# Optimization experiments

Hardware: AMD Instinct MI355X
Metric: run time of the kernel (lower is better)

## Reference

```python
import jax, jax.numpy as jnp
import numpy as np

EMB = 300      # node embedding dim (GNNGraph default)
NL = 5         # num GNN layers
G = 4096       # number of graphs in batch
ATOM_F, ATOM_V = 9, 128   # OGB-style atom encoder: 9 categorical feats
BOND_F, BOND_V = 3, 8     # OGB-style bond encoder: 3 categorical feats
BN_EPS = 1e-5


def _bn(x, g, b, m, v):
    # BatchNorm1d in eval mode (running stats)
    return (x - m) * jax.lax.rsqrt(v + BN_EPS) * g + b


def _gnn(x, edge_index, edge_attr, batch,
         atom_emb, bond_emb, vn_emb,
         gin_eps, gin_W1, gin_b1, gin_bn1_g, gin_bn1_b, gin_bn1_m, gin_bn1_v,
         gin_W2, gin_b2, bn_g, bn_b, bn_m, bn_v,
         vn_W1, vn_b1, vn_bn1_g, vn_bn1_b, vn_bn1_m, vn_bn1_v,
         vn_W2, vn_b2, vn_bn2_g, vn_bn2_b, vn_bn2_m, vn_bn2_v):
    N = x.shape[0]
    # AtomEncoder / BondEncoder: sum of per-feature embedding lookups
    h = atom_emb[jnp.arange(ATOM_F)[None, :], x].sum(axis=1)          # [N, EMB]
    e = bond_emb[jnp.arange(BOND_F)[None, :], edge_attr].sum(axis=1)  # [E, EMB]
    row, col = edge_index[0], edge_index[1]
    # virtual node embedding, one per graph
    vn = jnp.broadcast_to(vn_emb[0], (G, EMB))
    for l in range(NL):
        h = h + vn[batch]                                   # broadcast virtual node
        # GINConv: message = relu(x_j + edge_emb), aggr = scatter-add at target
        msg = jax.nn.relu(h[row] + e)                       # [E, EMB]
        agg = jax.ops.segment_sum(msg, col, num_segments=N) # [N, EMB]
        t = (1.0 + gin_eps[l]) * h + agg
        t = jnp.dot(t, gin_W1[l]) + gin_b1[l]               # [N, 2*EMB]
        t = jax.nn.relu(_bn(t, gin_bn1_g[l], gin_bn1_b[l], gin_bn1_m[l], gin_bn1_v[l]))
        t = jnp.dot(t, gin_W2[l]) + gin_b2[l]               # [N, EMB]
        hn = _bn(t, bn_g[l], bn_b[l], bn_m[l], bn_v[l])     # outer BatchNorm
        if l < NL - 1:
            hn = jax.nn.relu(hn)                            # (dropout inactive in eval)
            # virtual node update: global_add_pool(h_list[layer]) + vn -> MLP
            pooled = jax.ops.segment_sum(h, batch, num_segments=G) + vn
            u = jnp.dot(pooled, vn_W1[l]) + vn_b1[l]
            u = jax.nn.relu(_bn(u, vn_bn1_g[l], vn_bn1_b[l], vn_bn1_m[l], vn_bn1_v[l]))
            u = jnp.dot(u, vn_W2[l]) + vn_b2[l]
            vn = jax.nn.relu(_bn(u, vn_bn2_g[l], vn_bn2_b[l], vn_bn2_m[l], vn_bn2_v[l]))
        h = hn
    # global_mean_pool over graphs
    counts = jax.ops.segment_sum(jnp.ones((N,), h.dtype), batch, num_segments=G)
    return jax.ops.segment_sum(h, batch, num_segments=G) / jnp.maximum(counts, 1.0)[:, None]


def setup_inputs() -> dict:
    key = jax.random.key(0)
    ks = iter(jax.random.split(key, 64))
    N, E = 100000, 250000
    d = {}
    d['x'] = jax.random.randint(next(ks), (N, ATOM_F), 0, ATOM_V, dtype=jnp.int32)
    d['edge_index'] = jax.random.randint(next(ks), (2, E), 0, N, dtype=jnp.int32)
    d['edge_attr'] = jax.random.randint(next(ks), (E, BOND_F), 0, BOND_V, dtype=jnp.int32)
    d['batch'] = jnp.sort(jax.random.randint(next(ks), (N,), 0, G, dtype=jnp.int32))
    s = 0.05
    d['atom_emb'] = jax.random.normal(next(ks), (ATOM_F, ATOM_V, EMB), jnp.float32) * s
    d['bond_emb'] = jax.random.normal(next(ks), (BOND_F, BOND_V, EMB), jnp.float32) * s
    d['vn_emb'] = jax.random.normal(next(ks), (1, EMB), jnp.float32) * s
    d['gin_eps'] = jax.random.normal(next(ks), (NL,), jnp.float32) * 0.01
    d['gin_W1'] = jax.random.normal(next(ks), (NL, EMB, 2 * EMB), jnp.float32) * s
    d['gin_b1'] = jax.random.normal(next(ks), (NL, 2 * EMB), jnp.float32) * s
    d['gin_bn1_g'] = 1.0 + jax.random.normal(next(ks), (NL, 2 * EMB), jnp.float32) * s
    d['gin_bn1_b'] = jax.random.normal(next(ks), (NL, 2 * EMB), jnp.float32) * s
    d['gin_bn1_m'] = jax.random.normal(next(ks), (NL, 2 * EMB), jnp.float32) * s
    d['gin_bn1_v'] = jax.random.uniform(next(ks), (NL, 2 * EMB), jnp.float32) + 0.5
    d['gin_W2'] = jax.random.normal(next(ks), (NL, 2 * EMB, EMB), jnp.float32) * s
    d['gin_b2'] = jax.random.normal(next(ks), (NL, EMB), jnp.float32) * s
    d['bn_g'] = 1.0 + jax.random.normal(next(ks), (NL, EMB), jnp.float32) * s
    d['bn_b'] = jax.random.normal(next(ks), (NL, EMB), jnp.float32) * s
    d['bn_m'] = jax.random.normal(next(ks), (NL, EMB), jnp.float32) * s
    d['bn_v'] = jax.random.uniform(next(ks), (NL, EMB), jnp.float32) + 0.5
    V = NL - 1
    d['vn_W1'] = jax.random.normal(next(ks), (V, EMB, 2 * EMB), jnp.float32) * s
    d['vn_b1'] = jax.random.normal(next(ks), (V, 2 * EMB), jnp.float32) * s
    d['vn_bn1_g'] = 1.0 + jax.random.normal(next(ks), (V, 2 * EMB), jnp.float32) * s
    d['vn_bn1_b'] = jax.random.normal(next(ks), (V, 2 * EMB), jnp.float32) * s
    d['vn_bn1_m'] = jax.random.normal(next(ks), (V, 2 * EMB), jnp.float32) * s
    d['vn_bn1_v'] = jax.random.uniform(next(ks), (V, 2 * EMB), jnp.float32) + 0.5
    d['vn_W2'] = jax.random.normal(next(ks), (V, 2 * EMB, EMB), jnp.float32) * s
    d['vn_b2'] = jax.random.normal(next(ks), (V, EMB), jnp.float32) * s
    d['vn_bn2_g'] = 1.0 + jax.random.normal(next(ks), (V, EMB), jnp.float32) * s
    d['vn_bn2_b'] = jax.random.normal(next(ks), (V, EMB), jnp.float32) * s
    d['vn_bn2_m'] = jax.random.normal(next(ks), (V, EMB), jnp.float32) * s
    d['vn_bn2_v'] = jax.random.uniform(next(ks), (V, EMB), jnp.float32) + 0.5
    return d


def reference(x, edge_index, edge_attr, batch,
              atom_emb, bond_emb, vn_emb,
              gin_eps, gin_W1, gin_b1, gin_bn1_g, gin_bn1_b, gin_bn1_m, gin_bn1_v,
              gin_W2, gin_b2, bn_g, bn_b, bn_m, bn_v,
              vn_W1, vn_b1, vn_bn1_g, vn_bn1_b, vn_bn1_m, vn_bn1_v,
              vn_W2, vn_b2, vn_bn2_g, vn_bn2_b, vn_bn2_m, vn_bn2_v):
    return _gnn(x, edge_index, edge_attr, batch,
                atom_emb, bond_emb, vn_emb,
                gin_eps, gin_W1, gin_b1, gin_bn1_g, gin_bn1_b, gin_bn1_m, gin_bn1_v,
                gin_W2, gin_b2, bn_g, bn_b, bn_m, bn_v,
                vn_W1, vn_b1, vn_bn1_g, vn_bn1_b, vn_bn1_m, vn_bn1_v,
                vn_W2, vn_b2, vn_bn2_g, vn_bn2_b, vn_bn2_m, vn_bn2_v)
```

## Files before the change

### kernel.cpp

```cpp
#include <hip/hip_runtime.h>
#include <hip/hip_bf16.h>

#define EMBD 300
#define GG   4096
#define NLAY 5
#define KP1  320
#define KP2  640
#define NP1  640
#define NP2  384
#define WPER (NP1*KP1 + NP2*KP2)

typedef unsigned short ushort_t;
typedef short short8 __attribute__((ext_vector_type(8)));
typedef short short4v __attribute__((ext_vector_type(4)));
typedef float f32x4 __attribute__((ext_vector_type(4)));

static inline int cdiv(int a, int b) { return (a + b - 1) / b; }


__device__ inline void dma16(const ushort_t* g, ushort_t* l) {
    __builtin_amdgcn_global_load_lds(
        (const __attribute__((address_space(1))) unsigned int*)g,
        (__attribute__((address_space(3))) unsigned int*)l, 16, 0, 0);
}

__device__ inline ushort_t bf16_of(float v) {
    union { __hip_bfloat16 b; ushort_t u; } c;
    c.b = __float2bfloat16(v);
    return c.u;
}

__device__ inline float bf2f(ushort_t u) {
    union { unsigned int i; float f; } c;
    c.i = ((unsigned int)u) << 16;
    return c.f;
}


__global__ void atom_encode_bf(const int* __restrict__ x, const float* __restrict__ aemb,
                               ushort_t* __restrict__ h, int N) {
    int i = blockIdx.x * blockDim.x + threadIdx.x;
    int total = N * 75;
    if (i >= total) return;
    int n = i / 75, d4 = i - n * 75;
    const int* xr = x + n * 9;
    float4 s = make_float4(0.f, 0.f, 0.f, 0.f);
    const float4* a4 = (const float4*)aemb;
#pragma unroll
    for (int f = 0; f < 9; ++f) {
        float4 v = a4[(size_t)((f << 7) + xr[f]) * 75 + d4];
        s.x += v.x; s.y += v.y; s.z += v.z; s.w += v.w;
    }
    short4v o;
    o[0] = (short)bf16_of(s.x); o[1] = (short)bf16_of(s.y);
    o[2] = (short)bf16_of(s.z); o[3] = (short)bf16_of(s.w);
    *(short4v*)(h + (size_t)n * KP1 + d4 * 4) = o;
}

__global__ void init_vn4(const float* __restrict__ vn_emb, float* __restrict__ vn) {
    int i = blockIdx.x * blockDim.x + threadIdx.x;
    if (i >= GG * 75) return;
    ((float4*)vn)[i] = ((const float4*)vn_emb)[i % 75];
}

__global__ void find_starts(const int* __restrict__ batch, int* __restrict__ starts, int N) {
    int g = blockIdx.x * blockDim.x + threadIdx.x;
    if (g > GG) return;
    int lo = 0, hi = N;
    while (lo < hi) {
        int mid = (lo + hi) >> 1;
        if (batch[mid] < g) lo = mid + 1; else hi = mid;
    }
    starts[g] = lo;
}

__global__ void bond_combo(const float* __restrict__ bemb, float* __restrict__ ebsum) {
    int i = blockIdx.x * blockDim.x + threadIdx.x;
    if (i >= 512 * EMBD) return;
    int c = i / EMBD, d = i - c * EMBD;
    int a0 = c >> 6, a1 = (c >> 3) & 7, a2 = c & 7;
    ebsum[i] = bemb[a0 * EMBD + d] + bemb[(8 + a1) * EMBD + d] + bemb[(16 + a2) * EMBD + d];
}

__global__ void conv_all(const float* __restrict__ gW1, const float* __restrict__ gW2,
                         const float* __restrict__ vW1, const float* __restrict__ vW2,
                         ushort_t* __restrict__ wh) {
    int i = blockIdx.x * blockDim.x + threadIdx.x;
    int total = WPER * 9;
    if (i >= total) return;
    int mlp = i / WPER, r = i - mlp * WPER;
    const float *W1, *W2;
    if (mlp < NLAY) {
        W1 = gW1 + (size_t)mlp * EMBD * 2 * EMBD;
        W2 = gW2 + (size_t)mlp * 2 * EMBD * EMBD;
    } else {
        int l = mlp - NLAY;
        W1 = vW1 + (size_t)l * EMBD * 2 * EMBD;
        W2 = vW2 + (size_t)l * 2 * EMBD * EMBD;
    }
    float v;
    if (r < NP1 * KP1) {
        int n = r / KP1, k = r - n * KP1;
        v = (n < 2 * EMBD && k < EMBD) ? W1[(size_t)k * (2 * EMBD) + n] : 0.f;
    } else {
        int r2 = r - NP1 * KP1;
        int n = r2 / KP2, k = r2 - n * KP2;
        v = (n < EMBD && k < 2 * EMBD) ? W2[(size_t)k * EMBD + n] : 0.f;
    }
    wh[i] = bf16_of(v);
}


__global__ void ecount(const int* __restrict__ ei, int* __restrict__ cnt, int E) {
    int e = blockIdx.x * blockDim.x + threadIdx.x;
    if (e >= E) return;
    atomicAdd(&cnt[ei[E + e]], 1);
}

__global__ void scan_part(const int* __restrict__ cnt, int* __restrict__ bsum, int N) {
    __shared__ int sh[256];
    int b = blockIdx.x, t = threadIdx.x;
    int base = b * 1024;
    int s = 0;
    for (int j = t; j < 1024; j += 256) {
        int idx = base + j;
        if (idx < N) s += cnt[idx];
    }
    sh[t] = s;
    __syncthreads();
    for (int d = 128; d > 0; d >>= 1) {
        if (t < d) sh[t] += sh[t + d];
        __syncthreads();
    }
    if (t == 0) bsum[b] = sh[0];
}

__global__ void scan_top(int* __restrict__ bsum, int nb) {
    __shared__ int sh[1024];
    int t = threadIdx.x;
    int v = (t < nb) ? bsum[t] : 0;
    sh[t] = v;
    __syncthreads();
    for (int d = 1; d < 1024; d <<= 1) {
        int u = (t >= d) ? sh[t - d] : 0;
        __syncthreads();
        sh[t] += u;
        __syncthreads();
    }
    if (t < nb) bsum[t] = sh[t] - v;
}

__global__ void scan_final(const int* __restrict__ cnt, const int* __restrict__ bsum,
                           int* __restrict__ estart, int* __restrict__ cursor, int N, int E) {
    __shared__ int sh[256];
    int b = blockIdx.x, t = threadIdx.x;
    int base = b * 1024 + t * 4;
    int c[4];
    int s = 0;
#pragma unroll
    for (int j = 0; j < 4; ++j) {
        int idx = base + j;
        c[j] = (idx < N) ? cnt[idx] : 0;
        s += c[j];
    }
    sh[t] = s;
    __syncthreads();
    for (int d = 1; d < 256; d <<= 1) {
        int u = (t >= d) ? sh[t - d] : 0;
        __syncthreads();
        sh[t] += u;
        __syncthreads();
    }
    int run = sh[t] - s + bsum[b];
#pragma unroll
    for (int j = 0; j < 4; ++j) {
        int idx = base + j;
        if (idx < N) { estart[idx] = run; cursor[idx] = run; run += c[j]; }
    }
    if (b == 0 && t == 0) estart[N] = E;
}

__global__ void escatter(const int* __restrict__ ei, const int* __restrict__ ea,
                         int* __restrict__ cursor, int2* __restrict__ epack, int E) {
    int e = blockIdx.x * blockDim.x + threadIdx.x;
    if (e >= E) return;
    int c = ei[E + e];
    int p = atomicAdd(&cursor[c], 1);
    epack[p] = make_int2(ei[e], (ea[3 * e] << 6) | (ea[3 * e + 1] << 3) | ea[3 * e + 2]);
}


__global__ void pool_prep(ushort_t* __restrict__ h, const float* __restrict__ vn,
                          const int* __restrict__ starts, ushort_t* __restrict__ vnaB) {
    int g = blockIdx.x;
    int t = threadIdx.x;
    if (t >= EMBD) return;
    float vng = vn[(size_t)g * EMBD + t];
    int s0 = starts[g], s1 = starts[g + 1];
    float s = 0.f;
    for (int n = s0; n < s1; ++n) {
        size_t idx = (size_t)n * KP1 + t;
        float v = bf2f(h[idx]) + vng;
        h[idx] = bf16_of(v);
        s += v;
    }
    vnaB[(size_t)g * KP1 + t] = bf16_of(s + vng);
}

__global__ void prep_vn(ushort_t* __restrict__ h, const float* __restrict__ vn,
                        const int* __restrict__ batch, int N) {
    int i = blockIdx.x * blockDim.x + threadIdx.x;
    int total = N * 75;
    if (i >= total) return;
    int n = i / 75, d4 = i - n * 75;
    float4 vv = ((const float4*)vn)[(size_t)batch[n] * 75 + d4];
    short4v hv = *(short4v*)(h + (size_t)n * KP1 + d4 * 4);
    short4v o;
    o[0] = (short)bf16_of(bf2f((ushort_t)hv[0]) + vv.x);
    o[1] = (short)bf16_of(bf2f((ushort_t)hv[1]) + vv.y);
    o[2] = (short)bf16_of(bf2f((ushort_t)hv[2]) + vv.z);
    o[3] = (short)bf16_of(bf2f((ushort_t)hv[3]) + vv.w);
    *(short4v*)(h + (size_t)n * KP1 + d4 * 4) = o;
}

__global__ void pool_mean(const ushort_t* __restrict__ h, const int* __restrict__ starts,
                          float* __restrict__ out) {
    int g = blockIdx.x;
    int t = threadIdx.x;
    if (t >= EMBD) return;
    int s0 = starts[g], s1 = starts[g + 1];
    float s = 0.f;
    for (int n = s0; n < s1; ++n) s += bf2f(h[(size_t)n * KP1 + t]);
    float cnt = (float)(s1 - s0);
    out[(size_t)g * EMBD + t] = s / fmaxf(cnt, 1.0f);
}

#define NPB 4

__global__ void aggregate(const ushort_t* __restrict__ h, const float* __restrict__ ebsum,
                          const int* __restrict__ estart, const int2* __restrict__ epack,
                          const float* __restrict__ epsp,
                          ushort_t* __restrict__ aggB, int N) {
    int n = blockIdx.x * NPB + threadIdx.x / 80;
    int slot = threadIdx.x % 80;
    if (n >= N) return;
    float4 acc = make_float4(0.f, 0.f, 0.f, 0.f);
    if (slot < 75) {
        const float4* b4 = (const float4*)ebsum;
        float ce = 1.0f + *epsp;
        short4v hv = *(const short4v*)(h + (size_t)n * KP1 + slot * 4);
        acc.x = ce * bf2f((ushort_t)hv[0]);
        acc.y = ce * bf2f((ushort_t)hv[1]);
        acc.z = ce * bf2f((ushort_t)hv[2]);
        acc.w = ce * bf2f((ushort_t)hv[3]);
        int p0 = estart[n], p1 = estart[n + 1];
        for (int p = p0; p < p1; ++p) {
            int2 ep = epack[p];
            short4v xv = *(const short4v*)(h + (size_t)ep.x * KP1 + slot * 4);
            float4 ev = b4[(size_t)ep.y * 75 + slot];
            acc.x += fmaxf(bf2f((ushort_t)xv[0]) + ev.x, 0.f);
            acc.y += fmaxf(bf2f((ushort_t)xv[1]) + ev.y, 0.f);
            acc.z += fmaxf(bf2f((ushort_t)xv[2]) + ev.z, 0.f);
            acc.w += fmaxf(bf2f((ushort_t)xv[3]) + ev.w, 0.f);
        }
    }
    short4v bv4;
    bv4[0] = (short)bf16_of(acc.x);
    bv4[1] = (short)bf16_of(acc.y);
    bv4[2] = (short)bf16_of(acc.z);
    bv4[3] = (short)bf16_of(acc.w);
    *(short4v*)(aggB + (size_t)n * KP1 + slot * 4) = bv4;
}

#define BMg 128
#define BNg 128

__global__ __launch_bounds__(256) void gemm_as(
    const ushort_t* __restrict__ A, int KP,
    const ushort_t* __restrict__ B,
    const float* __restrict__ bias, const float* __restrict__ gg,
    const float* __restrict__ bb, const float* __restrict__ bm,
    const float* __restrict__ bv,
    int Mc, int NnReal, int relu, int nb, int mb,
    float* __restrict__ outF, int ldF,
    ushort_t* __restrict__ outB, int ldP)
{
    __shared__ ushort_t sA[2][BMg * 32];
    __shared__ ushort_t sB[2][BNg * 32];

    int id = blockIdx.x;
    int hi = id / (8 * nb);
    int rem = id - hi * 8 * nb;
    int xcd = rem & 7;
    int nblk = rem >> 3;
    int mblk = hi * 8 + xcd;
    if (mblk >= mb) return;

    const int tid = threadIdx.x;
    const int lane = tid & 63;
    const int w = tid >> 6;
    const int m0 = mblk * BMg;
    const int n0 = nblk * BNg;
    const int wm = (w & 1) * 64;
    const int wn = (w >> 1) * 64;

    const ushort_t* gA[2];
    const ushort_t* gB[2];
    int lbase[2];
#pragma unroll
    for (int i = 0; i < 2; ++i) {
        int s = tid + 256 * i;
        int m = s >> 2, qp = s & 3;
        int q = (qp - (m >> 1)) & 3;
        int msrc = (m0 + m < Mc) ? (m0 + m) : (Mc - 1);
        gA[i] = A + (size_t)msrc * KP + 8 * q;
        gB[i] = B + (size_t)(n0 + m) * KP + 8 * q;
        lbase[i] = (w * 64 + 256 * i) * 8;
    }

    f32x4 acc[4][4];
#pragma unroll
    for (int a = 0; a < 4; ++a)
#pragma unroll
        for (int b = 0; b < 4; ++b) acc[a][b] = (f32x4)(0.f);

    const int q = lane >> 4;
    const int c16 = lane & 15;
    const int kt = KP >> 5;

#pragma unroll
    for (int i = 0; i < 2; ++i) {
        dma16(gA[i], sA[0] + lbase[i]); gA[i] += 32;
        dma16(gB[i], sB[0] + lbase[i]); gB[i] += 32;
    }
    __syncthreads();

    for (int t = 0; t < kt; ++t) {
        int cur = t & 1, nxt = cur ^ 1;
        if (t + 1 < kt) {
#pragma unroll
            for (int i = 0; i < 2; ++i) {
                dma16(gA[i], sA[nxt] + lbase[i]); gA[i] += 32;
                dma16(gB[i], sB[nxt] + lbase[i]); gB[i] += 32;
            }
        }
        short8 av[4], bhv[4];
#pragma unroll
        for (int tt = 0; tt < 4; ++tt) {
            int m = wm + tt * 16 + c16;
            int q2 = (q + (m >> 1)) & 3;
            av[tt] = *(const short8*)(sA[cur] + m * 32 + q2 * 8);
        }
#pragma unroll
        for (int uu = 0; uu < 4; ++uu) {
            int n = wn + uu * 16 + c16;
            int q2 = (q + (n >> 1)) & 3;
            bhv[uu] = *(const short8*)(sB[cur] + n * 32 + q2 * 8);
        }
#pragma unroll
        for (int tt = 0; tt < 4; ++tt)
#pragma unroll
            for (int uu = 0; uu < 4; ++uu)
                acc[tt][uu] = __builtin_amdgcn_mfma_f32_16x16x32_bf16(av[tt], bhv[uu], acc[tt][uu], 0, 0, 0);
        __syncthreads();
    }

#pragma unroll
    for (int uu = 0; uu < 4; ++uu) {
        int gn = n0 + wn + uu * 16 + c16;
        float sc = 0.f, sh = 0.f;
        if (gn < NnReal) {
            sc = gg[gn] * rsqrtf(bv[gn] + 1e-5f);
            sh = bb[gn] + (bias[gn] - bm[gn]) * sc;
        }
#pragma unroll
        for (int tt = 0; tt < 4; ++tt) {
            int rbase = m0 + wm + tt * 16 + q * 4;
#pragma unroll
            for (int r = 0; r < 4; ++r) {
                int gm = rbase + r;
                if (gm >= Mc) continue;
                float y = acc[tt][uu][r] * sc + sh;
                if (relu) y = fmaxf(y, 0.f);
                if (outF) {
                    if (gn < NnReal) outF[(size_t)gm * ldF + gn] = y;
                } else {
                    if (gn < ldP) outB[(size_t)gm * ldP + gn] = bf16_of(y);
                }
            }
        }
    }
}


struct MlpP {
    const float *b1, *g1, *be1, *m1, *v1;
    const float *b2, *g2, *be2, *m2, *v2;
};

static void run_mlp(hipStream_t stream, const ushort_t* inB, int M,
                    const ushort_t* wh, int mlp,
                    ushort_t* tB, int CH,
                    const MlpP& W, ushort_t* outB, int relu2) {
    const ushort_t* w1 = wh + (size_t)mlp * WPER;
    const ushort_t* w2 = w1 + NP1 * KP1;
    for (int c0 = 0; c0 < M; c0 += CH) {
        int Mc = (M - c0 < CH) ? (M - c0) : CH;
        int mb = cdiv(Mc, BMg);
        int mbp = cdiv(mb, 8) * 8;
        {
            int nb = NP1 / BNg;
            gemm_as<<<nb * mbp, 256, 0, stream>>>(
                inB + (size_t)c0 * KP1, KP1, w1,
                W.b1, W.g1, W.be1, W.m1, W.v1,
                Mc, 2 * EMBD, 1, nb, mb,
                nullptr, 0, tB, KP2);
        }
        {
            int nb = NP2 / BNg;
            gemm_as<<<nb * mbp, 256, 0, stream>>>(
                tB, KP2, w2,
                W.b2, W.g2, W.be2, W.m2, W.v2,
                Mc, EMBD, relu2, nb, mb,
                nullptr, 0, outB + (size_t)c0 * KP1, KP1);
        }
    }
}


extern "C" void kernel_launch(void* const* d_in, const int* in_sizes, int n_in,
                              void* d_out, int out_size, void* d_ws, size_t ws_size,
                              hipStream_t stream) {
    const int*   x        = (const int*)d_in[0];
    const int*   ei       = (const int*)d_in[1];
    const int*   ea       = (const int*)d_in[2];
    const int*   batch    = (const int*)d_in[3];
    const float* atom_emb = (const float*)d_in[4];
    const float* bond_emb = (const float*)d_in[5];
    const float* vn_emb   = (const float*)d_in[6];
    const float* gin_eps  = (const float*)d_in[7];
    const float* gin_W1   = (const float*)d_in[8];
    const float* gin_b1   = (const float*)d_in[9];
    const float* gin_bn1g = (const float*)d_in[10];
    const float* gin_bn1b = (const float*)d_in[11];
    const float* gin_bn1m = (const float*)d_in[12];
    const float* gin_bn1v = (const float*)d_in[13];
    const float* gin_W2   = (const float*)d_in[14];
    const float* gin_b2   = (const float*)d_in[15];
    const float* bn_g     = (const float*)d_in[16];
    const float* bn_b     = (const float*)d_in[17];
    const float* bn_m     = (const float*)d_in[18];
    const float* bn_v     = (const float*)d_in[19];
    const float* vn_W1    = (const float*)d_in[20];
    const float* vn_b1    = (const float*)d_in[21];
    const float* vn_bn1g  = (const float*)d_in[22];
    const float* vn_bn1b  = (const float*)d_in[23];
    const float* vn_bn1m  = (const float*)d_in[24];
    const float* vn_bn1v  = (const float*)d_in[25];
    const float* vn_W2    = (const float*)d_in[26];
    const float* vn_b2    = (const float*)d_in[27];
    const float* vn_bn2g  = (const float*)d_in[28];
    const float* vn_bn2b  = (const float*)d_in[29];
    const float* vn_bn2m  = (const float*)d_in[30];
    const float* vn_bn2v  = (const float*)d_in[31];

    const int N = in_sizes[3];
    const int E = in_sizes[1] / 2;
    const int NB = cdiv(N, 1024);

    char* base = (char*)d_ws;
    size_t off = 0;
    ushort_t* hbuf = (ushort_t*)(base + off); off += (size_t)N * KP1 * 2;
    ushort_t* aggB = (ushort_t*)(base + off); off += (size_t)N * KP1 * 2;
    float* vnbuf   = (float*)(base + off);    off += (size_t)GG * EMBD * 4;
    int*   starts  = (int*)(base + off);      off += 4104 * 4;
    int*   cnt     = (int*)(base + off);      off += (size_t)N * 4;
    int*   cursor  = (int*)(base + off);      off += (size_t)N * 4;
    int*   estart  = (int*)(base + off);      off += ((size_t)N + 8) * 4;
    int*   bsum    = (int*)(base + off);      off += 1032 * 4;
    int2*  epack   = (int2*)(base + off);     off += (size_t)E * 8;
    float* ebsum   = (float*)(base + off);    off += (size_t)512 * EMBD * 4;
    ushort_t* whA  = (ushort_t*)(base + off); off += (size_t)9 * WPER * 2;
    ushort_t* vnaB = (ushort_t*)(base + off); off += (size_t)GG * KP1 * 2;
    off = (off + 255) & ~(size_t)255;

    size_t avail = (ws_size > off) ? ws_size - off : 0;
    int CH = (int)(avail / (KP2 * 2));
    CH &= ~255;
    if (CH > N) CH = (N + 255) & ~255;
    else if (CH >= (N + 1) / 2) CH = (((N + 1) / 2) + 255) & ~255;
    if (CH < 2048) CH = 2048;
    ushort_t* tB = (ushort_t*)(base + off);

    const int BLK = 256;
    int ne4 = N * 75;

    find_starts<<<cdiv(GG + 1, BLK), BLK, 0, stream>>>(batch, starts, N);
    atom_encode_bf<<<cdiv(ne4, BLK), BLK, 0, stream>>>(x, atom_emb, hbuf, N);
    init_vn4<<<cdiv(GG * 75, BLK), BLK, 0, stream>>>(vn_emb, vnbuf);
    bond_combo<<<cdiv(512 * EMBD, BLK), BLK, 0, stream>>>(bond_emb, ebsum);
    conv_all<<<cdiv(9 * WPER, BLK), BLK, 0, stream>>>(gin_W1, gin_W2, vn_W1, vn_W2, whA);
    hipMemsetAsync(cnt, 0, (size_t)N * 4, stream);
    hipMemsetAsync(vnaB, 0, (size_t)GG * KP1 * 2, stream);
    ecount<<<cdiv(E, BLK), BLK, 0, stream>>>(ei, cnt, E);
    scan_part<<<NB, 256, 0, stream>>>(cnt, bsum, N);
    scan_top<<<1, 1024, 0, stream>>>(bsum, NB);
    scan_final<<<NB, 256, 0, stream>>>(cnt, bsum, estart, cursor, N, E);
    escatter<<<cdiv(E, BLK), BLK, 0, stream>>>(ei, ea, cursor, epack, E);

    for (int l = 0; l < NLAY; ++l) {
        int last = (l == NLAY - 1);

        if (!last)
            pool_prep<<<GG, 320, 0, stream>>>(hbuf, vnbuf, starts, vnaB);
        else
            prep_vn<<<cdiv(ne4, BLK), BLK, 0, stream>>>(hbuf, vnbuf, batch, N);

        aggregate<<<cdiv(N, NPB), NPB * 80, 0, stream>>>(
            hbuf, ebsum, estart, epack, gin_eps + l, aggB, N);

        MlpP Wn = { gin_b1 + (size_t)l * 2 * EMBD,
                    gin_bn1g + (size_t)l * 2 * EMBD, gin_bn1b + (size_t)l * 2 * EMBD,
                    gin_bn1m + (size_t)l * 2 * EMBD, gin_bn1v + (size_t)l * 2 * EMBD,
                    gin_b2 + (size_t)l * EMBD,
                    bn_g + (size_t)l * EMBD, bn_b + (size_t)l * EMBD,
                    bn_m + (size_t)l * EMBD, bn_v + (size_t)l * EMBD };
        run_mlp(stream, aggB, N, whA, l, tB, CH, Wn, hbuf, last ? 0 : 1);

        if (!last) {
            MlpP Wv = { vn_b1 + (size_t)l * 2 * EMBD,
                        vn_bn1g + (size_t)l * 2 * EMBD, vn_bn1b + (size_t)l * 2 * EMBD,
                        vn_bn1m + (size_t)l * 2 * EMBD, vn_bn1v + (size_t)l * 2 * EMBD,
                        vn_b2 + (size_t)l * EMBD,
                        vn_bn2g + (size_t)l * EMBD, vn_bn2b + (size_t)l * EMBD,
                        vn_bn2m + (size_t)l * EMBD, vn_bn2v + (size_t)l * EMBD };
            const ushort_t* w1 = whA + (size_t)(NLAY + l) * WPER;
            const ushort_t* w2 = w1 + NP1 * KP1;
            int mb = cdiv(GG, BMg), mbp = cdiv(mb, 8) * 8;
            gemm_as<<<(NP1 / BNg) * mbp, 256, 0, stream>>>(
                vnaB, KP1, w1,
                Wv.b1, Wv.g1, Wv.be1, Wv.m1, Wv.v1,
                GG, 2 * EMBD, 1, NP1 / BNg, mb,
                nullptr, 0, tB, KP2);
            gemm_as<<<(NP2 / BNg) * mbp, 256, 0, stream>>>(
                tB, KP2, w2,
                Wv.b2, Wv.g2, Wv.be2, Wv.m2, Wv.v2,
                GG, EMBD, 1, NP2 / BNg, mb,
                vnbuf, EMBD, nullptr, 0);
        }
    }

    pool_mean<<<GG, 320, 0, stream>>>(hbuf, starts, (float*)d_out);
}
```

Baseline: 1.933 ms.

## Fuse two-layer MLP GEMMs into one kernel and fold virtual-node add into epilogue

```diff
diff --git a/kernel.cpp b/kernel.cpp
--- a/kernel.cpp
+++ b/kernel.cpp
@@ -38,13 +38,14 @@
 
 
 __global__ void atom_encode_bf(const int* __restrict__ x, const float* __restrict__ aemb,
+                               const float* __restrict__ vn_emb,
                                ushort_t* __restrict__ h, int N) {
     int i = blockIdx.x * blockDim.x + threadIdx.x;
     int total = N * 75;
     if (i >= total) return;
     int n = i / 75, d4 = i - n * 75;
     const int* xr = x + n * 9;
-    float4 s = make_float4(0.f, 0.f, 0.f, 0.f);
+    float4 s = ((const float4*)vn_emb)[d4];
     const float4* a4 = (const float4*)aemb;
 #pragma unroll
     for (int f = 0; f < 9; ++f) {
@@ -190,37 +191,15 @@
 }
 
 
-__global__ void pool_prep(ushort_t* __restrict__ h, const float* __restrict__ vn,
+__global__ void pool_only(const ushort_t* __restrict__ h, const float* __restrict__ vn,
                           const int* __restrict__ starts, ushort_t* __restrict__ vnaB) {
     int g = blockIdx.x;
     int t = threadIdx.x;
     if (t >= EMBD) return;
-    float vng = vn[(size_t)g * EMBD + t];
     int s0 = starts[g], s1 = starts[g + 1];
     float s = 0.f;
-    for (int n = s0; n < s1; ++n) {
-        size_t idx = (size_t)n * KP1 + t;
-        float v = bf2f(h[idx]) + vng;
-        h[idx] = bf16_of(v);
-        s += v;
-    }
-    vnaB[(size_t)g * KP1 + t] = bf16_of(s + vng);
-}
-
-__global__ void prep_vn(ushort_t* __restrict__ h, const float* __restrict__ vn,
-                        const int* __restrict__ batch, int N) {
-    int i = blockIdx.x * blockDim.x + threadIdx.x;
-    int total = N * 75;
-    if (i >= total) return;
-    int n = i / 75, d4 = i - n * 75;
-    float4 vv = ((const float4*)vn)[(size_t)batch[n] * 75 + d4];
-    short4v hv = *(short4v*)(h + (size_t)n * KP1 + d4 * 4);
-    short4v o;
-    o[0] = (short)bf16_of(bf2f((ushort_t)hv[0]) + vv.x);
-    o[1] = (short)bf16_of(bf2f((ushort_t)hv[1]) + vv.y);
-    o[2] = (short)bf16_of(bf2f((ushort_t)hv[2]) + vv.z);
-    o[3] = (short)bf16_of(bf2f((ushort_t)hv[3]) + vv.w);
-    *(short4v*)(h + (size_t)n * KP1 + d4 * 4) = o;
+    for (int n = s0; n < s1; ++n) s += bf2f(h[(size_t)n * KP1 + t]);
+    vnaB[(size_t)g * KP1 + t] = bf16_of(s + vn[(size_t)g * EMBD + t]);
 }
 
 __global__ void pool_mean(const ushort_t* __restrict__ h, const int* __restrict__ starts,
@@ -272,159 +251,147 @@
     *(short4v*)(aggB + (size_t)n * KP1 + slot * 4) = bv4;
 }
 
-#define BMg 128
-#define BNg 128
-
-__global__ __launch_bounds__(256) void gemm_as(
-    const ushort_t* __restrict__ A, int KP,
-    const ushort_t* __restrict__ B,
-    const float* __restrict__ bias, const float* __restrict__ gg,
-    const float* __restrict__ bb, const float* __restrict__ bm,
-    const float* __restrict__ bv,
-    int Mc, int NnReal, int relu, int nb, int mb,
-    float* __restrict__ outF, int ldF,
-    ushort_t* __restrict__ outB, int ldP)
+
+__global__ __launch_bounds__(256, 2) void fused_mlp(
+    const ushort_t* __restrict__ A,
+    const ushort_t* __restrict__ W1,
+    const ushort_t* __restrict__ W2,
+    const float* __restrict__ b1, const float* __restrict__ g1,
+    const float* __restrict__ bb1, const float* __restrict__ bm1, const float* __restrict__ bv1,
+    const float* __restrict__ b2, const float* __restrict__ g2,
+    const float* __restrict__ bb2, const float* __restrict__ bm2, const float* __restrict__ bv2,
+    int M, int relu2,
+    const float* __restrict__ vnadd, const int* __restrict__ batch,
+    ushort_t* __restrict__ outB,
+    float* __restrict__ outF)
 {
-    __shared__ ushort_t sA[2][BMg * 32];
-    __shared__ ushort_t sB[2][BNg * 32];
-
-    int id = blockIdx.x;
-    int hi = id / (8 * nb);
-    int rem = id - hi * 8 * nb;
-    int xcd = rem & 7;
-    int nblk = rem >> 3;
-    int mblk = hi * 8 + xcd;
-    if (mblk >= mb) return;
+    __shared__ ushort_t sA[10 * 64 * 32];
+    __shared__ ushort_t tL[64 * 136];
 
     const int tid = threadIdx.x;
     const int lane = tid & 63;
     const int w = tid >> 6;
-    const int m0 = mblk * BMg;
-    const int n0 = nblk * BNg;
-    const int wm = (w & 1) * 64;
-    const int wn = (w >> 1) * 64;
-
-    const ushort_t* gA[2];
-    const ushort_t* gB[2];
-    int lbase[2];
-#pragma unroll
-    for (int i = 0; i < 2; ++i) {
-        int s = tid + 256 * i;
-        int m = s >> 2, qp = s & 3;
-        int q = (qp - (m >> 1)) & 3;
-        int msrc = (m0 + m < Mc) ? (m0 + m) : (Mc - 1);
-        gA[i] = A + (size_t)msrc * KP + 8 * q;
-        gB[i] = B + (size_t)(n0 + m) * KP + 8 * q;
-        lbase[i] = (w * 64 + 256 * i) * 8;
-    }
-
-    f32x4 acc[4][4];
-#pragma unroll
-    for (int a = 0; a < 4; ++a)
-#pragma unroll
-        for (int b = 0; b < 4; ++b) acc[a][b] = (f32x4)(0.f);
-
+    const int m0 = blockIdx.x * 64;
     const int q = lane >> 4;
     const int c16 = lane & 15;
-    const int kt = KP >> 5;
-
-#pragma unroll
-    for (int i = 0; i < 2; ++i) {
-        dma16(gA[i], sA[0] + lbase[i]); gA[i] += 32;
-        dma16(gB[i], sB[0] + lbase[i]); gB[i] += 32;
+
+    {
+        int m = tid >> 2, qp = tid & 3;
+        int q0 = (qp - (m >> 1)) & 3;
+        int msrc = m0 + m; if (msrc >= M) msrc = M - 1;
+        const ushort_t* gA = A + (size_t)msrc * KP1 + 8 * q0;
+        int lb = w * 512;
+#pragma unroll
+        for (int kt = 0; kt < 10; ++kt)
+            dma16(gA + kt * 32, sA + kt * 2048 + lb);
     }
     __syncthreads();
 
-    for (int t = 0; t < kt; ++t) {
-        int cur = t & 1, nxt = cur ^ 1;
-        if (t + 1 < kt) {
-#pragma unroll
-            for (int i = 0; i < 2; ++i) {
-                dma16(gA[i], sA[nxt] + lbase[i]); gA[i] += 32;
-                dma16(gB[i], sB[nxt] + lbase[i]); gB[i] += 32;
+    f32x4 acc2[4][6];
+#pragma unroll
+    for (int a = 0; a < 4; ++a)
+#pragma unroll
+        for (int b = 0; b < 6; ++b) acc2[a][b] = (f32x4)(0.f);
+
+    for (int c = 0; c < 5; ++c) {
+        float sc1[2], sh1[2];
+#pragma unroll
+        for (int uu = 0; uu < 2; ++uu) {
+            int col = c * 128 + w * 32 + uu * 16 + c16;
+            if (col < 2 * EMBD) {
+                float s = g1[col] * rsqrtf(bv1[col] + 1e-5f);
+                sc1[uu] = s;
+                sh1[uu] = bb1[col] + (b1[col] - bm1[col]) * s;
+            } else { sc1[uu] = 0.f; sh1[uu] = 0.f; }
+        }
+        f32x4 acc1[4][2];
+#pragma unroll
+        for (int a = 0; a < 4; ++a) { acc1[a][0] = (f32x4)(0.f); acc1[a][1] = (f32x4)(0.f); }
+        for (int kt = 0; kt < 10; ++kt) {
+            short8 bf[2];
+#pragma unroll
+            for (int uu = 0; uu < 2; ++uu) {
+                int ncol = c * 128 + w * 32 + uu * 16 + c16;
+                bf[uu] = *(const short8*)(W1 + (size_t)ncol * KP1 + kt * 32 + q * 8);
             }
-        }
-        short8 av[4], bhv[4];
-#pragma unroll
-        for (int tt = 0; tt < 4; ++tt) {
-            int m = wm + tt * 16 + c16;
-            int q2 = (q + (m >> 1)) & 3;
-            av[tt] = *(const short8*)(sA[cur] + m * 32 + q2 * 8);
-        }
-#pragma unroll
-        for (int uu = 0; uu < 4; ++uu) {
-            int n = wn + uu * 16 + c16;
-            int q2 = (q + (n >> 1)) & 3;
-            bhv[uu] = *(const short8*)(sB[cur] + n * 32 + q2 * 8);
-        }
-#pragma unroll
-        for (int tt = 0; tt < 4; ++tt)
-#pragma unroll
-            for (int uu = 0; uu < 4; ++uu)
-                acc[tt][uu] = __builtin_amdgcn_mfma_f32_16x16x32_bf16(av[tt], bhv[uu], acc[tt][uu], 0, 0, 0);
-        __syncthreads();
-    }
-
-#pragma unroll
-    for (int uu = 0; uu < 4; ++uu) {
-        int gn = n0 + wn + uu * 16 + c16;
-        float sc = 0.f, sh = 0.f;
-        if (gn < NnReal) {
-            sc = gg[gn] * rsqrtf(bv[gn] + 1e-5f);
-            sh = bb[gn] + (bias[gn] - bm[gn]) * sc;
-        }
-#pragma unroll
-        for (int tt = 0; tt < 4; ++tt) {
-            int rbase = m0 + wm + tt * 16 + q * 4;
-#pragma unroll
-            for (int r = 0; r < 4; ++r) {
-                int gm = rbase + r;
-                if (gm >= Mc) continue;
-                float y = acc[tt][uu][r] * sc + sh;
-                if (relu) y = fmaxf(y, 0.f);
-                if (outF) {
-                    if (gn < NnReal) outF[(size_t)gm * ldF + gn] = y;
+            short8 af[4];
+#pragma unroll
+            for (int tt = 0; tt < 4; ++tt) {
+                int m2 = tt * 16 + c16;
+                int q2 = (q + (m2 >> 1)) & 3;
+                af[tt] = *(const short8*)(sA + kt * 2048 + m2 * 32 + q2 * 8);
+            }
+#pragma unroll
+            for (int tt = 0; tt < 4; ++tt)
+#pragma unroll
+                for (int uu = 0; uu < 2; ++uu)
+                    acc1[tt][uu] = __builtin_amdgcn_mfma_f32_16x16x32_bf16(af[tt], bf[uu], acc1[tt][uu], 0, 0, 0);
+        }
+#pragma unroll
+        for (int uu = 0; uu < 2; ++uu) {
+            int col = w * 32 + uu * 16 + c16;
+#pragma unroll
+            for (int tt = 0; tt < 4; ++tt)
+#pragma unroll
+                for (int r = 0; r < 4; ++r) {
+                    int row = tt * 16 + q * 4 + r;
+                    float y = fmaxf(acc1[tt][uu][r] * sc1[uu] + sh1[uu], 0.f);
+                    tL[row * 136 + col] = bf16_of(y);
+                }
+        }
+        __syncthreads();
+        for (int kt2 = 0; kt2 < 4; ++kt2) {
+            short8 bf2[6];
+#pragma unroll
+            for (int uu = 0; uu < 6; ++uu) {
+                int ncol = w * 96 + uu * 16 + c16;
+                bf2[uu] = *(const short8*)(W2 + (size_t)ncol * KP2 + c * 128 + kt2 * 32 + q * 8);
+            }
+            short8 af2[4];
+#pragma unroll
+            for (int tt = 0; tt < 4; ++tt) {
+                int m2 = tt * 16 + c16;
+                af2[tt] = *(const short8*)(tL + m2 * 136 + kt2 * 32 + q * 8);
+            }
+#pragma unroll
+            for (int tt = 0; tt < 4; ++tt)
+#pragma unroll
+                for (int uu = 0; uu < 6; ++uu)
+                    acc2[tt][uu] = __builtin_amdgcn_mfma_f32_16x16x32_bf16(af2[tt], bf2[uu], acc2[tt][uu], 0, 0, 0);
+        }
+        __syncthreads();
+    }
+
+    float sc2[6], sh2[6];
+#pragma unroll
+    for (int uu = 0; uu < 6; ++uu) {
+        int gn = w * 96 + uu * 16 + c16;
+        if (gn < EMBD) {
+            float s = g2[gn] * rsqrtf(bv2[gn] + 1e-5f);
+            sc2[uu] = s;
+            sh2[uu] = bb2[gn] + (b2[gn] - bm2[gn]) * s;
+        } else { sc2[uu] = 0.f; sh2[uu] = 0.f; }
+    }
+#pragma unroll
+    for (int tt = 0; tt < 4; ++tt)
+#pragma unroll
+        for (int r = 0; r < 4; ++r) {
+            int gm = m0 + tt * 16 + q * 4 + r;
+            if (gm >= M) continue;
+            const float* vrow = vnadd ? (vnadd + (size_t)batch[gm] * EMBD) : nullptr;
+#pragma unroll
+            for (int uu = 0; uu < 6; ++uu) {
+                int gn = w * 96 + uu * 16 + c16;
+                float y = acc2[tt][uu][r] * sc2[uu] + sh2[uu];
+                if (relu2) y = fmaxf(y, 0.f);
+                if (vrow && gn < EMBD) y += vrow[gn];
+                if (outB) {
+                    if (gn < KP1) outB[(size_t)gm * KP1 + gn] = bf16_of(y);
                 } else {
-                    if (gn < ldP) outB[(size_t)gm * ldP + gn] = bf16_of(y);
+                    if (gn < EMBD) outF[(size_t)gm * EMBD + gn] = y;
                 }
             }
         }
-    }
-}
-
-
-struct MlpP {
-    const float *b1, *g1, *be1, *m1, *v1;
-    const float *b2, *g2, *be2, *m2, *v2;
-};
-
-static void run_mlp(hipStream_t stream, const ushort_t* inB, int M,
-                    const ushort_t* wh, int mlp,
-                    ushort_t* tB, int CH,
-                    const MlpP& W, ushort_t* outB, int relu2) {
-    const ushort_t* w1 = wh + (size_t)mlp * WPER;
-    const ushort_t* w2 = w1 + NP1 * KP1;
-    for (int c0 = 0; c0 < M; c0 += CH) {
-        int Mc = (M - c0 < CH) ? (M - c0) : CH;
-        int mb = cdiv(Mc, BMg);
-        int mbp = cdiv(mb, 8) * 8;
-        {
-            int nb = NP1 / BNg;
-            gemm_as<<<nb * mbp, 256, 0, stream>>>(
-                inB + (size_t)c0 * KP1, KP1, w1,
-                W.b1, W.g1, W.be1, W.m1, W.v1,
-                Mc, 2 * EMBD, 1, nb, mb,
-                nullptr, 0, tB, KP2);
-        }
-        {
-            int nb = NP2 / BNg;
-            gemm_as<<<nb * mbp, 256, 0, stream>>>(
-                tB, KP2, w2,
-                W.b2, W.g2, W.be2, W.m2, W.v2,
-                Mc, EMBD, relu2, nb, mb,
-                nullptr, 0, outB + (size_t)c0 * KP1, KP1);
-        }
-    }
 }
 
 
@@ -482,21 +449,12 @@
     float* ebsum   = (float*)(base + off);    off += (size_t)512 * EMBD * 4;
     ushort_t* whA  = (ushort_t*)(base + off); off += (size_t)9 * WPER * 2;
     ushort_t* vnaB = (ushort_t*)(base + off); off += (size_t)GG * KP1 * 2;
-    off = (off + 255) & ~(size_t)255;
-
-    size_t avail = (ws_size > off) ? ws_size - off : 0;
-    int CH = (int)(avail / (KP2 * 2));
-    CH &= ~255;
-    if (CH > N) CH = (N + 255) & ~255;
-    else if (CH >= (N + 1) / 2) CH = (((N + 1) / 2) + 255) & ~255;
-    if (CH < 2048) CH = 2048;
-    ushort_t* tB = (ushort_t*)(base + off);
 
     const int BLK = 256;
     int ne4 = N * 75;
 
     find_starts<<<cdiv(GG + 1, BLK), BLK, 0, stream>>>(batch, starts, N);
-    atom_encode_bf<<<cdiv(ne4, BLK), BLK, 0, stream>>>(x, atom_emb, hbuf, N);
+    atom_encode_bf<<<cdiv(ne4, BLK), BLK, 0, stream>>>(x, atom_emb, vn_emb, hbuf, N);
     init_vn4<<<cdiv(GG * 75, BLK), BLK, 0, stream>>>(vn_emb, vnbuf);
     bond_combo<<<cdiv(512 * EMBD, BLK), BLK, 0, stream>>>(bond_emb, ebsum);
     conv_all<<<cdiv(9 * WPER, BLK), BLK, 0, stream>>>(gin_W1, gin_W2, vn_W1, vn_W2, whA);
@@ -511,42 +469,39 @@
     for (int l = 0; l < NLAY; ++l) {
         int last = (l == NLAY - 1);
 
-        if (!last)
-            pool_prep<<<GG, 320, 0, stream>>>(hbuf, vnbuf, starts, vnaB);
-        else
-            prep_vn<<<cdiv(ne4, BLK), BLK, 0, stream>>>(hbuf, vnbuf, batch, N);
+        if (!last) {
+            pool_only<<<GG, 320, 0, stream>>>(hbuf, vnbuf, starts, vnaB);
+            const ushort_t* w1 = whA + (size_t)(NLAY + l) * WPER;
+            const ushort_t* w2 = w1 + NP1 * KP1;
+            fused_mlp<<<cdiv(GG, 64), 256, 0, stream>>>(
+                vnaB, w1, w2,
+                vn_b1 + (size_t)l * 2 * EMBD, vn_bn1g + (size_t)l * 2 * EMBD,
+                vn_bn1b + (size_t)l * 2 * EMBD, vn_bn1m + (size_t)l * 2 * EMBD,
+                vn_bn1v + (size_t)l * 2 * EMBD,
+                vn_b2 + (size_t)l * EMBD, vn_bn2g + (size_t)l * EMBD,
+                vn_bn2b + (size_t)l * EMBD, vn_bn2m + (size_t)l * EMBD,
+                vn_bn2v + (size_t)l * EMBD,
+                GG, 1, nullptr, nullptr,
+                nullptr, vnbuf);
+        }
 
         aggregate<<<cdiv(N, NPB), NPB * 80, 0, stream>>>(
             hbuf, ebsum, estart, epack, gin_eps + l, aggB, N);
 
-        MlpP Wn = { gin_b1 + (size_t)l * 2 * EMBD,
-                    gin_bn1g + (size_t)l * 2 * EMBD, gin_bn1b + (size_t)l * 2 * EMBD,
-                    gin_bn1m + (size_t)l * 2 * EMBD, gin_bn1v + (size_t)l * 2 * EMBD,
-                    gin_b2 + (size_t)l * EMBD,
-                    bn_g + (size_t)l * EMBD, bn_b + (size_t)l * EMBD,
-                    bn_m + (size_t)l * EMBD, bn_v + (size_t)l * EMBD };
-        run_mlp(stream, aggB, N, whA, l, tB, CH, Wn, hbuf, last ? 0 : 1);
-
-        if (!last) {
-            MlpP Wv = { vn_b1 + (size_t)l * 2 * EMBD,
-                        vn_bn1g + (size_t)l * 2 * EMBD, vn_bn1b + (size_t)l * 2 * EMBD,
-                        vn_bn1m + (size_t)l * 2 * EMBD, vn_bn1v + (size_t)l * 2 * EMBD,
-                        vn_b2 + (size_t)l * EMBD,
-                        vn_bn2g + (size_t)l * EMBD, vn_bn2b + (size_t)l * EMBD,
-                        vn_bn2m + (size_t)l * EMBD, vn_bn2v + (size_t)l * EMBD };
-            const ushort_t* w1 = whA + (size_t)(NLAY + l) * WPER;
+        {
+            const ushort_t* w1 = whA + (size_t)l * WPER;
             const ushort_t* w2 = w1 + NP1 * KP1;
-            int mb = cdiv(GG, BMg), mbp = cdiv(mb, 8) * 8;
-            gemm_as<<<(NP1 / BNg) * mbp, 256, 0, stream>>>(
-                vnaB, KP1, w1,
-                Wv.b1, Wv.g1, Wv.be1, Wv.m1, Wv.v1,
-                GG, 2 * EMBD, 1, NP1 / BNg, mb,
-                nullptr, 0, tB, KP2);
-            gemm_as<<<(NP2 / BNg) * mbp, 256, 0, stream>>>(
-                tB, KP2, w2,
-                Wv.b2, Wv.g2, Wv.be2, Wv.m2, Wv.v2,
-                GG, EMBD, 1, NP2 / BNg, mb,
-                vnbuf, EMBD, nullptr, 0);
+            fused_mlp<<<cdiv(N, 64), 256, 0, stream>>>(
+                aggB, w1, w2,
+                gin_b1 + (size_t)l * 2 * EMBD, gin_bn1g + (size_t)l * 2 * EMBD,
+                gin_bn1b + (size_t)l * 2 * EMBD, gin_bn1m + (size_t)l * 2 * EMBD,
+                gin_bn1v + (size_t)l * 2 * EMBD,
+                gin_b2 + (size_t)l * EMBD, bn_g + (size_t)l * EMBD,
+                bn_b + (size_t)l * EMBD, bn_m + (size_t)l * EMBD,
+                bn_v + (size_t)l * EMBD,
+                N, last ? 0 : 1,
+                last ? nullptr : vnbuf, batch,
+                hbuf, nullptr);
         }
     }
 
```

After: 2.258 ms. 16.8% more time.

## Fold virtual-node broadcast into node-MLP epilogue and make pooling read-only

Applied to the files above, without the earlier changes.

```diff
diff --git a/kernel.cpp b/kernel.cpp
--- a/kernel.cpp
+++ b/kernel.cpp
@@ -38,13 +38,14 @@
 
 
 __global__ void atom_encode_bf(const int* __restrict__ x, const float* __restrict__ aemb,
+                               const float* __restrict__ vn_emb,
                                ushort_t* __restrict__ h, int N) {
     int i = blockIdx.x * blockDim.x + threadIdx.x;
     int total = N * 75;
     if (i >= total) return;
     int n = i / 75, d4 = i - n * 75;
     const int* xr = x + n * 9;
-    float4 s = make_float4(0.f, 0.f, 0.f, 0.f);
+    float4 s = ((const float4*)vn_emb)[d4];
     const float4* a4 = (const float4*)aemb;
 #pragma unroll
     for (int f = 0; f < 9; ++f) {
@@ -190,37 +191,15 @@
 }
 
 
-__global__ void pool_prep(ushort_t* __restrict__ h, const float* __restrict__ vn,
+__global__ void pool_only(const ushort_t* __restrict__ h, const float* __restrict__ vn,
                           const int* __restrict__ starts, ushort_t* __restrict__ vnaB) {
     int g = blockIdx.x;
     int t = threadIdx.x;
     if (t >= EMBD) return;
-    float vng = vn[(size_t)g * EMBD + t];
     int s0 = starts[g], s1 = starts[g + 1];
     float s = 0.f;
-    for (int n = s0; n < s1; ++n) {
-        size_t idx = (size_t)n * KP1 + t;
-        float v = bf2f(h[idx]) + vng;
-        h[idx] = bf16_of(v);
-        s += v;
-    }
-    vnaB[(size_t)g * KP1 + t] = bf16_of(s + vng);
-}
-
-__global__ void prep_vn(ushort_t* __restrict__ h, const float* __restrict__ vn,
-                        const int* __restrict__ batch, int N) {
-    int i = blockIdx.x * blockDim.x + threadIdx.x;
-    int total = N * 75;
-    if (i >= total) return;
-    int n = i / 75, d4 = i - n * 75;
-    float4 vv = ((const float4*)vn)[(size_t)batch[n] * 75 + d4];
-    short4v hv = *(short4v*)(h + (size_t)n * KP1 + d4 * 4);
-    short4v o;
-    o[0] = (short)bf16_of(bf2f((ushort_t)hv[0]) + vv.x);
-    o[1] = (short)bf16_of(bf2f((ushort_t)hv[1]) + vv.y);
-    o[2] = (short)bf16_of(bf2f((ushort_t)hv[2]) + vv.z);
-    o[3] = (short)bf16_of(bf2f((ushort_t)hv[3]) + vv.w);
-    *(short4v*)(h + (size_t)n * KP1 + d4 * 4) = o;
+    for (int n = s0; n < s1; ++n) s += bf2f(h[(size_t)n * KP1 + t]);
+    vnaB[(size_t)g * KP1 + t] = bf16_of(s + vn[(size_t)g * EMBD + t]);
 }
 
 __global__ void pool_mean(const ushort_t* __restrict__ h, const int* __restrict__ starts,
@@ -282,6 +261,7 @@
     const float* __restrict__ bb, const float* __restrict__ bm,
     const float* __restrict__ bv,
     int Mc, int NnReal, int relu, int nb, int mb,
+    const float* __restrict__ vnadd, const int* __restrict__ batchp,
     float* __restrict__ outF, int ldF,
     ushort_t* __restrict__ outB, int ldP)
 {
@@ -365,23 +345,29 @@
         __syncthreads();
     }
 
+    float sc[4], sh[4];
 #pragma unroll
     for (int uu = 0; uu < 4; ++uu) {
         int gn = n0 + wn + uu * 16 + c16;
-        float sc = 0.f, sh = 0.f;
         if (gn < NnReal) {
-            sc = gg[gn] * rsqrtf(bv[gn] + 1e-5f);
-            sh = bb[gn] + (bias[gn] - bm[gn]) * sc;
-        }
-#pragma unroll
-        for (int tt = 0; tt < 4; ++tt) {
-            int rbase = m0 + wm + tt * 16 + q * 4;
-#pragma unroll
-            for (int r = 0; r < 4; ++r) {
-                int gm = rbase + r;
-                if (gm >= Mc) continue;
-                float y = acc[tt][uu][r] * sc + sh;
+            float s = gg[gn] * rsqrtf(bv[gn] + 1e-5f);
+            sc[uu] = s;
+            sh[uu] = bb[gn] + (bias[gn] - bm[gn]) * s;
+        } else { sc[uu] = 0.f; sh[uu] = 0.f; }
+    }
+#pragma unroll
+    for (int tt = 0; tt < 4; ++tt)
+#pragma unroll
+        for (int r = 0; r < 4; ++r) {
+            int gm = m0 + wm + tt * 16 + q * 4 + r;
+            if (gm >= Mc) continue;
+            const float* vrow = vnadd ? (vnadd + (size_t)batchp[gm] * EMBD) : nullptr;
+#pragma unroll
+            for (int uu = 0; uu < 4; ++uu) {
+                int gn = n0 + wn + uu * 16 + c16;
+                float y = acc[tt][uu][r] * sc[uu] + sh[uu];
                 if (relu) y = fmaxf(y, 0.f);
+                if (vrow && gn < EMBD) y += vrow[gn];
                 if (outF) {
                     if (gn < NnReal) outF[(size_t)gm * ldF + gn] = y;
                 } else {
@@ -389,7 +375,6 @@
                 }
             }
         }
-    }
 }
 
 
@@ -401,7 +386,8 @@
 static void run_mlp(hipStream_t stream, const ushort_t* inB, int M,
                     const ushort_t* wh, int mlp,
                     ushort_t* tB, int CH,
-                    const MlpP& W, ushort_t* outB, int relu2) {
+                    const MlpP& W, ushort_t* outB, int relu2,
+                    const float* vnadd, const int* batch) {
     const ushort_t* w1 = wh + (size_t)mlp * WPER;
     const ushort_t* w2 = w1 + NP1 * KP1;
     for (int c0 = 0; c0 < M; c0 += CH) {
@@ -414,6 +400,7 @@
                 inB + (size_t)c0 * KP1, KP1, w1,
                 W.b1, W.g1, W.be1, W.m1, W.v1,
                 Mc, 2 * EMBD, 1, nb, mb,
+                nullptr, nullptr,
                 nullptr, 0, tB, KP2);
         }
         {
@@ -422,6 +409,7 @@
                 tB, KP2, w2,
                 W.b2, W.g2, W.be2, W.m2, W.v2,
                 Mc, EMBD, relu2, nb, mb,
+                vnadd, vnadd ? (batch + c0) : nullptr,
                 nullptr, 0, outB + (size_t)c0 * KP1, KP1);
         }
     }
@@ -496,7 +484,7 @@
     int ne4 = N * 75;
 
     find_starts<<<cdiv(GG + 1, BLK), BLK, 0, stream>>>(batch, starts, N);
-    atom_encode_bf<<<cdiv(ne4, BLK), BLK, 0, stream>>>(x, atom_emb, hbuf, N);
+    atom_encode_bf<<<cdiv(ne4, BLK), BLK, 0, stream>>>(x, atom_emb, vn_emb, hbuf, N);
     init_vn4<<<cdiv(GG * 75, BLK), BLK, 0, stream>>>(vn_emb, vnbuf);
     bond_combo<<<cdiv(512 * EMBD, BLK), BLK, 0, stream>>>(bond_emb, ebsum);
     conv_all<<<cdiv(9 * WPER, BLK), BLK, 0, stream>>>(gin_W1, gin_W2, vn_W1, vn_W2, whA);
@@ -511,10 +499,28 @@
     for (int l = 0; l < NLAY; ++l) {
         int last = (l == NLAY - 1);
 
-        if (!last)
-            pool_prep<<<GG, 320, 0, stream>>>(hbuf, vnbuf, starts, vnaB);
-        else
-            prep_vn<<<cdiv(ne4, BLK), BLK, 0, stream>>>(hbuf, vnbuf, batch, N);
+        if (!last) {
+            pool_only<<<GG, 320, 0, stream>>>(hbuf, vnbuf, starts, vnaB);
+            const ushort_t* w1 = whA + (size_t)(NLAY + l) * WPER;
+            const ushort_t* w2 = w1 + NP1 * KP1;
+            int mb = cdiv(GG, BMg), mbp = cdiv(mb, 8) * 8;
+            gemm_as<<<(NP1 / BNg) * mbp, 256, 0, stream>>>(
+                vnaB, KP1, w1,
+                vn_b1 + (size_t)l * 2 * EMBD, vn_bn1g + (size_t)l * 2 * EMBD,
+                vn_bn1b + (size_t)l * 2 * EMBD, vn_bn1m + (size_t)l * 2 * EMBD,
+                vn_bn1v + (size_t)l * 2 * EMBD,
+                GG, 2 * EMBD, 1, NP1 / BNg, mb,
+                nullptr, nullptr,
+                nullptr, 0, tB, KP2);
+            gemm_as<<<(NP2 / BNg) * mbp, 256, 0, stream>>>(
+                tB, KP2, w2,
+                vn_b2 + (size_t)l * EMBD, vn_bn2g + (size_t)l * EMBD,
+                vn_bn2b + (size_t)l * EMBD, vn_bn2m + (size_t)l * EMBD,
+                vn_bn2v + (size_t)l * EMBD,
+                GG, EMBD, 1, NP2 / BNg, mb,
+                nullptr, nullptr,
+                vnbuf, EMBD, nullptr, 0);
+        }
 
         aggregate<<<cdiv(N, NPB), NPB * 80, 0, stream>>>(
             hbuf, ebsum, estart, epack, gin_eps + l, aggB, N);
@@ -525,29 +531,8 @@
                     gin_b2 + (size_t)l * EMBD,
                     bn_g + (size_t)l * EMBD, bn_b + (size_t)l * EMBD,
                     bn_m + (size_t)l * EMBD, bn_v + (size_t)l * EMBD };
-        run_mlp(stream, aggB, N, whA, l, tB, CH, Wn, hbuf, last ? 0 : 1);
-
-        if (!last) {
-            MlpP Wv = { vn_b1 + (size_t)l * 2 * EMBD,
-                        vn_bn1g + (size_t)l * 2 * EMBD, vn_bn1b + (size_t)l * 2 * EMBD,
-                        vn_bn1m + (size_t)l * 2 * EMBD, vn_bn1v + (size_t)l * 2 * EMBD,
-                        vn_b2 + (size_t)l * EMBD,
-                        vn_bn2g + (size_t)l * EMBD, vn_bn2b + (size_t)l * EMBD,
-                        vn_bn2m + (size_t)l * EMBD, vn_bn2v + (size_t)l * EMBD };
-            const ushort_t* w1 = whA + (size_t)(NLAY + l) * WPER;
-            const ushort_t* w2 = w1 + NP1 * KP1;
-            int mb = cdiv(GG, BMg), mbp = cdiv(mb, 8) * 8;
-            gemm_as<<<(NP1 / BNg) * mbp, 256, 0, stream>>>(
-                vnaB, KP1, w1,
-                Wv.b1, Wv.g1, Wv.be1, Wv.m1, Wv.v1,
-                GG, 2 * EMBD, 1, NP1 / BNg, mb,
-                nullptr, 0, tB, KP2);
-            gemm_as<<<(NP2 / BNg) * mbp, 256, 0, stream>>>(
-                tB, KP2, w2,
-                Wv.b2, Wv.g2, Wv.be2, Wv.m2, Wv.v2,
-                GG, EMBD, 1, NP2 / BNg, mb,
-                vnbuf, EMBD, nullptr, 0);
-        }
+        run_mlp(stream, aggB, N, whA, l, tB, CH, Wn, hbuf, last ? 0 : 1,
+                last ? nullptr : vnbuf, batch);
     }
 
     pool_mean<<<GG, 320, 0, stream>>>(hbuf, starts, (float*)d_out);
```

Result: slower. 2.137 ms (+10.6%).
